# Performance work log

Hardware: AMD Instinct MI355X
Metric: run time of the kernel (lower is better)

The kernel has to match this reference:

```python
import jax, jax.numpy as jnp
import numpy as np

N_HEADS = 16
HEAD_SIZE = 64
N_EMB = 1024
BLOCK = 2048
B, T = 2, 2048

def setup_inputs() -> dict:
    key = jax.random.key(0)
    ks = jax.random.split(key, 6)
    s = 0.02
    x = jax.random.normal(ks[0], (B, T, N_EMB), dtype=jnp.float32)
    # per-head projection weights, stacked: [H, C, hs] (no bias, per module)
    Wq = jax.random.normal(ks[1], (N_HEADS, N_EMB, HEAD_SIZE), dtype=jnp.float32) * s
    Wk = jax.random.normal(ks[2], (N_HEADS, N_EMB, HEAD_SIZE), dtype=jnp.float32) * s
    Wv = jax.random.normal(ks[3], (N_HEADS, N_EMB, HEAD_SIZE), dtype=jnp.float32) * s
    # output projection: Linear(n_heads*head_size -> n_embedding), with bias
    Wo = jax.random.normal(ks[4], (N_HEADS * HEAD_SIZE, N_EMB), dtype=jnp.float32) * s
    bo = jax.random.normal(ks[5], (N_EMB,), dtype=jnp.float32) * s
    return {"x": x, "Wq": Wq, "Wk": Wk, "Wv": Wv, "Wo": Wo, "bo": bo}

def reference(x, Wq, Wk, Wv, Wo, bo):
    # x: [B,T,C]; projections per head -> [B,H,T,hs]
    q = jnp.einsum('btc,hcd->bhtd', x, Wq)
    k = jnp.einsum('btc,hcd->bhtd', x, Wk)
    v = jnp.einsum('btc,hcd->bhtd', x, Wv)
    scale = 1.0 / jnp.sqrt(jnp.asarray(HEAD_SIZE, dtype=x.dtype))
    scores = jnp.einsum('bhtd,bhsd->bhts', q, k) * scale  # [B,H,T,T]
    Tq = x.shape[1]
    causal = jnp.tril(jnp.ones((Tq, Tq), dtype=bool))
    scores = jnp.where(causal, scores, jnp.asarray(-jnp.inf, dtype=scores.dtype))
    attn = jax.nn.softmax(scores, axis=-1)  # dropout in eval mode (identity)
    out = jnp.einsum('bhts,bhsd->bhtd', attn, v)  # [B,H,T,hs]
    # concat heads along last dim (matches torch.cat order over head list)
    out = out.transpose(0, 2, 1, 3).reshape(x.shape[0], Tq, N_HEADS * HEAD_SIZE)
    return out @ Wo + bo
```

## Files before the change

### kernel.cpp

```cpp
#include <hip/hip_runtime.h>


typedef short v8s __attribute__((ext_vector_type(8)));
typedef float v4f __attribute__((ext_vector_type(4)));

#define DEVI __device__ __forceinline__

#define B_SZ 2
#define T_SEQ 2048
#define NH 16
#define HS 64
#define CEMB 1024
#define MROWS (B_SZ * T_SEQ)
#define KSZ 1024
#define SCALE_Q 0.18033688011112042f

DEVI unsigned short f2bf(float f) {
  union { float f; unsigned u; } c; c.f = f;
  unsigned u = c.u;
  unsigned r = (u + 0x7FFFu + ((u >> 16) & 1u)) >> 16;
  return (unsigned short)r;
}

DEVI float exp2_fast(float x) {
  float r;
  asm("v_exp_f32 %0, %1" : "=v"(r) : "v"(x));
  return r;
}

DEVI unsigned cvt_pk_bf16(float lo, float hi) {
  unsigned r;
  asm("v_cvt_pk_bf16_f32 %0, %1, %2" : "=v"(r) : "v"(lo), "v"(hi));
  return r;
}

DEVI void gload_lds16(const void* g, void* l) {
  __builtin_amdgcn_global_load_lds(
      (const __attribute__((address_space(1))) void*)g,
      (__attribute__((address_space(3))) void*)l, 16, 0, 0);
}

DEVI int xcd_swz(int bid, int nwg) {
  int q = nwg >> 3;
  return (bid & 7) * q + (bid >> 3);
}

__global__ __launch_bounds__(256, 4) void prep_kernel(
    const float* __restrict__ x, const float* __restrict__ Wq,
    const float* __restrict__ Wk, const float* __restrict__ Wv,
    const float* __restrict__ Wo, unsigned short* __restrict__ xb,
    unsigned short* __restrict__ Wt, unsigned short* __restrict__ Wot) {
  int bid = blockIdx.x;
  if (bid < 2048) {
    int i = bid * 2048 + threadIdx.x * 8;
    float4 a = *(const float4*)(x + i);
    float4 b = *(const float4*)(x + i + 4);
    ushort4 o0, o1;
    o0.x = f2bf(a.x); o0.y = f2bf(a.y); o0.z = f2bf(a.z); o0.w = f2bf(a.w);
    o1.x = f2bf(b.x); o1.y = f2bf(b.y); o1.z = f2bf(b.z); o1.w = f2bf(b.w);
    *(ushort4*)(xb + i) = o0;
    *(ushort4*)(xb + i + 4) = o1;
    return;
  }
  __shared__ float tile[32][33];
  const float* in; unsigned short* out;
  int C, bx, by;
  if (bid < 5120) {
    int b2 = bid - 2048;
    int widx = b2 >> 10, rem = b2 & 1023;
    in = (widx == 0 ? Wq : (widx == 1 ? Wk : Wv));
    int z = rem >> 6;
    bx = rem & 1; by = (rem >> 1) & 31;
    C = 64;
    in += (size_t)z * 1024 * 64;
    out = Wt + ((size_t)widx << 20) + (size_t)z * 1024 * 64;
  } else {
    int rem = bid - 5120;
    C = 1024;
    bx = rem & 31; by = rem >> 5;
    in = Wo; out = Wot;
  }
  int c0 = bx * 32, r0 = by * 32;
  int tx = threadIdx.x & 31, ty = threadIdx.x >> 5;
#pragma unroll
  for (int j = 0; j < 4; ++j)
    tile[ty + j * 8][tx] = in[(size_t)(r0 + ty + j * 8) * C + c0 + tx];
  __syncthreads();
#pragma unroll
  for (int j = 0; j < 4; ++j)
    out[(size_t)(c0 + ty + j * 8) * 1024 + r0 + tx] = f2bf(tile[tx][ty + j * 8]);
}

__global__ __launch_bounds__(256, 3) void gemm_qkv(
    const unsigned short* __restrict__ A, const unsigned short* __restrict__ Bt,
    unsigned short* __restrict__ Cout, int nbx) {
  __shared__ __align__(16) unsigned char lds[49152];
  unsigned short* As = (unsigned short*)lds;
  unsigned short* Bs = (unsigned short*)(lds + 24576);

  const int tid = threadIdx.x;
  const int lane = tid & 63, w = tid >> 6;
  const int wm = w >> 1, wn = w & 1;
  const int lr = lane & 15, lg = lane >> 4;

  const int wg = xcd_swz(blockIdx.x, gridDim.x);
  const int mb = (wg / nbx) * 128, nb = (wg % nbx) * 128;

  v4f acc[4][4];
  v4f zero = {0.f, 0.f, 0.f, 0.f};
#pragma unroll
  for (int i = 0; i < 4; ++i)
#pragma unroll
    for (int j = 0; j < 4; ++j) acc[i][j] = zero;

  const int srow = lane >> 2;
  const int sgcol = ((lane & 3) ^ (srow & 3)) * 8;
  const unsigned short* gA = A + (size_t)(mb + w * 32 + srow) * KSZ + sgcol;
  const unsigned short* gB = Bt + (size_t)(nb + w * 32 + srow) * KSZ + sgcol;
  unsigned short* lA = As + w * 1024;
  unsigned short* lB = Bs + w * 1024;

#define STAGE_G(buf, kb)                                        \
  do {                                                          \
    gload_lds16(gA + (kb), lA + (buf) * 4096);                  \
    gload_lds16(gA + (kb) + 16 * KSZ, lA + (buf) * 4096 + 512); \
    gload_lds16(gB + (kb), lB + (buf) * 4096);                  \
    gload_lds16(gB + (kb) + 16 * KSZ, lB + (buf) * 4096 + 512); \
  } while (0)

  STAGE_G(0, 0);
  STAGE_G(1, 32);
  STAGE_G(2, 64);

  const int NT = KSZ / 32;
  for (int t = 0; t < NT; ++t) {
    if (t < NT - 2)
      asm volatile("s_waitcnt vmcnt(8)" ::: "memory");
    else if (t == NT - 2)
      asm volatile("s_waitcnt vmcnt(4)" ::: "memory");
    else
      asm volatile("s_waitcnt vmcnt(0)" ::: "memory");
    __builtin_amdgcn_s_barrier();

    const int buf = t % 3;
    v8s af[4], bfr[4];
#pragma unroll
    for (int i = 0; i < 4; ++i) {
      int ra = wm * 64 + i * 16 + lr, rb = wn * 64 + i * 16 + lr;
      af[i]  = *(const v8s*)&As[buf * 4096 + ra * 32 + ((lg ^ (lr & 3)) << 3)];
      bfr[i] = *(const v8s*)&Bs[buf * 4096 + rb * 32 + ((lg ^ (lr & 3)) << 3)];
    }
#pragma unroll
    for (int i = 0; i < 4; ++i)
#pragma unroll
      for (int j = 0; j < 4; ++j)
        acc[i][j] = __builtin_amdgcn_mfma_f32_16x16x32_bf16(af[i], bfr[j], acc[i][j], 0, 0, 0);

    asm volatile("s_waitcnt lgkmcnt(0)" ::: "memory");
    __builtin_amdgcn_s_barrier();
    if (t + 3 < NT) STAGE_G(buf, (t + 3) * 32);
  }
#undef STAGE_G

  if ((wg % nbx) >= 16) {
    unsigned short* out = (unsigned short*)Cout;
#pragma unroll
    for (int i = 0; i < 4; ++i) {
      int tl0 = wm * 64 + i * 16 + lg * 4;
      int tc = tl0 >> 3, off = (tl0 & 7) * 2;
#pragma unroll
      for (int j = 0; j < 4; ++j) {
        int dl = wn * 64 + j * 16 + lr;
        unsigned lo = cvt_pk_bf16(acc[i][j][0], acc[i][j][1]);
        unsigned hi = cvt_pk_bf16(acc[i][j][2], acc[i][j][3]);
        unsigned char* p = lds + dl * 256 + ((tc ^ (dl & 15)) << 4) + off;
        *(unsigned*)p = lo;
        *(unsigned*)(p + 4) = hi;
      }
    }
    __syncthreads();
    int b = mb >> 11, mt = mb & 2047;
    int nrem0 = nb & 1023;
    unsigned short* Vg = out + (size_t)(2 * B_SZ * NH) * T_SEQ * HS;
#pragma unroll
    for (int it = 0; it < 8; ++it) {
      int dl = it * 16 + (tid >> 4);
      int tc = tid & 15;
      const unsigned char* p = lds + dl * 256 + ((tc ^ (dl & 15)) << 4);
      int4 vv = *(const int4*)p;
      int nrem = nrem0 + dl;
      int h = nrem >> 6, dd = nrem & 63;
      *(int4*)(Vg + ((size_t)(b * NH + h) * HS + dd) * T_SEQ + mt + tc * 8) = vv;
    }
    return;
  }

#pragma unroll
  for (int i = 0; i < 4; ++i) {
    int mrow0 = mb + wm * 64 + i * 16 + lg * 4;
#pragma unroll
    for (int j = 0; j < 4; ++j) {
      int ncol = nb + wn * 64 + j * 16 + lr;
      int p = ncol >> 10, rem = ncol & 1023, h = rem >> 6, d = rem & 63;
      float sc = (p == 0) ? SCALE_Q : 1.0f;
      unsigned short* out = (unsigned short*)Cout;
#pragma unroll
      for (int r = 0; r < 4; ++r) {
        int mrow = mrow0 + r;
        int b = mrow >> 11, t = mrow & 2047;
        out[((size_t)((p * B_SZ + b) * NH + h) * T_SEQ + t) * HS + d] =
            f2bf(acc[i][j][r] * sc);
      }
    }
  }
}

__global__ __launch_bounds__(256, 4) void gemm_proj(
    const unsigned short* __restrict__ A, const unsigned short* __restrict__ Bt,
    float* __restrict__ Cout, const float* __restrict__ bias, int nbx) {
  __shared__ __align__(16) unsigned short As[3][64 * 32];
  __shared__ __align__(16) unsigned short Bs[3][128 * 32];

  const int tid = threadIdx.x;
  const int lane = tid & 63, w = tid >> 6;
  const int wm = w >> 1, wn = w & 1;
  const int lr = lane & 15, lg = lane >> 4;

  const int wg = xcd_swz(blockIdx.x, gridDim.x);
  const int mb = (wg / nbx) * 64, nb = (wg % nbx) * 128;

  v4f acc[2][4];
  v4f zero = {0.f, 0.f, 0.f, 0.f};
#pragma unroll
  for (int i = 0; i < 2; ++i)
#pragma unroll
    for (int j = 0; j < 4; ++j) acc[i][j] = zero;

  const int srow = lane >> 2;
  const int sgcol = ((lane & 3) ^ (srow & 3)) * 8;
  const unsigned short* gA = A + (size_t)(mb + w * 16 + srow) * KSZ + sgcol;
  const unsigned short* gB = Bt + (size_t)(nb + w * 32 + srow) * KSZ + sgcol;
  unsigned short* lA = &As[0][0] + w * 512;
  unsigned short* lB = &Bs[0][0] + w * 1024;

#define STAGE_P(buf, kb)                                        \
  do {                                                          \
    gload_lds16(gA + (kb), lA + (buf) * 2048);                  \
    gload_lds16(gB + (kb), lB + (buf) * 4096);                  \
    gload_lds16(gB + (kb) + 16 * KSZ, lB + (buf) * 4096 + 512); \
  } while (0)

  STAGE_P(0, 0);
  STAGE_P(1, 32);
  STAGE_P(2, 64);

  const int NT = KSZ / 32;
  for (int t = 0; t < NT; ++t) {
    if (t < NT - 2)
      asm volatile("s_waitcnt vmcnt(6)" ::: "memory");
    else if (t == NT - 2)
      asm volatile("s_waitcnt vmcnt(3)" ::: "memory");
    else
      asm volatile("s_waitcnt vmcnt(0)" ::: "memory");
    __builtin_amdgcn_s_barrier();

    const int buf = t % 3;
    v8s af[2], bfr[4];
#pragma unroll
    for (int i = 0; i < 2; ++i) {
      int ra = wm * 32 + i * 16 + lr;
      af[i] = *(const v8s*)&As[buf][ra * 32 + ((lg ^ (lr & 3)) << 3)];
    }
#pragma unroll
    for (int j = 0; j < 4; ++j) {
      int rb = wn * 64 + j * 16 + lr;
      bfr[j] = *(const v8s*)&Bs[buf][rb * 32 + ((lg ^ (lr & 3)) << 3)];
    }
#pragma unroll
    for (int i = 0; i < 2; ++i)
#pragma unroll
      for (int j = 0; j < 4; ++j)
        acc[i][j] = __builtin_amdgcn_mfma_f32_16x16x32_bf16(af[i], bfr[j], acc[i][j], 0, 0, 0);

    asm volatile("s_waitcnt lgkmcnt(0)" ::: "memory");
    __builtin_amdgcn_s_barrier();
    if (t + 3 < NT) STAGE_P(buf, (t + 3) * 32);
  }
#undef STAGE_P

#pragma unroll
  for (int i = 0; i < 2; ++i) {
    int mrow0 = mb + wm * 32 + i * 16 + lg * 4;
#pragma unroll
    for (int j = 0; j < 4; ++j) {
      int ncol = nb + wn * 64 + j * 16 + lr;
      float bv = bias[ncol];
#pragma unroll
      for (int r = 0; r < 4; ++r)
        Cout[(size_t)(mrow0 + r) * CEMB + ncol] = acc[i][j][r] + bv;
    }
  }
}

__global__ __launch_bounds__(256, 4) void attn_kernel(
    const unsigned short* __restrict__ Qg, const unsigned short* __restrict__ Kg,
    const unsigned short* __restrict__ Vtg, unsigned short* __restrict__ Yg) {
  __shared__ __align__(16) unsigned char lds[32 * 1024];
  unsigned char* KsB = lds;
  unsigned char* VtB = lds + 16384;

  const int tid = threadIdx.x;
  const int lane = tid & 63, w = tid >> 6;
  const int lr = lane & 15, lg = lane >> 4;
  const int qc = 31 - (blockIdx.x >> 5);
  const int bh = blockIdx.x & 31;

  const unsigned short* Qbase = Qg + (size_t)bh * T_SEQ * HS;
  const unsigned short* Kbase = Kg + (size_t)bh * T_SEQ * HS;
  const unsigned short* Vtbase = Vtg + (size_t)bh * T_SEQ * HS;

  const int ks_row = tid >> 1, ks_c0 = (tid & 1) * 4;
  const unsigned short* Kg0 = Kbase + ks_row * HS + ks_c0 * 8;
  const int vs_d = tid >> 3, m0 = (tid & 7) * 2;
  const int vbt0 = ((m0 >> 2) << 4) + ((m0 & 3) << 2);
  const unsigned short* Vg0 = Vtbase + (size_t)vs_d * T_SEQ + vbt0;

  v8s qA[2];
  {
    const unsigned short* qrow = Qbase + (size_t)(qc * 64 + w * 16 + lr) * HS;
    qA[0] = *(const v8s*)(qrow + lg * 8);
    qA[1] = *(const v8s*)(qrow + 32 + lg * 8);
  }

  v4f O[4];
  v4f zero = {0.f, 0.f, 0.f, 0.f};
#pragma unroll
  for (int d = 0; d < 4; ++d) O[d] = zero;
  float mrun = -1e30f, lrun = 0.f;

  const int td = qc >> 1, oddq = qc & 1;

  int4 kA0 = ((const int4*)Kg0)[0], kA1 = ((const int4*)Kg0)[1];
  int4 kA2 = ((const int4*)Kg0)[2], kA3 = ((const int4*)Kg0)[3];
  int4 vl0 = *(const int4*)(Vg0);
  int4 vh0 = *(const int4*)(Vg0 + 64);
  int4 vl1 = *(const int4*)(Vg0 + 32 * T_SEQ);
  int4 vh1 = *(const int4*)(Vg0 + 32 * T_SEQ + 64);

  for (int t = 0; t <= td; ++t) {
    __syncthreads();
    {
      unsigned char* kp = KsB + ks_row * 128;
      *(int4*)(kp + (((ks_c0 + 0) ^ (ks_row & 7)) << 4)) = kA0;
      *(int4*)(kp + (((ks_c0 + 1) ^ (ks_row & 7)) << 4)) = kA1;
      *(int4*)(kp + (((ks_c0 + 2) ^ (ks_row & 7)) << 4)) = kA2;
      *(int4*)(kp + (((ks_c0 + 3) ^ (ks_row & 7)) << 4)) = kA3;
      int4 w0; w0.x = vl0.x; w0.y = vl0.y; w0.z = vh0.x; w0.w = vh0.y;
      int4 w1; w1.x = vl0.z; w1.y = vl0.w; w1.z = vh0.z; w1.w = vh0.w;
      unsigned char* vp = VtB + vs_d * 256;
      *(int4*)(vp + ((m0 ^ (vs_d & 15)) << 4)) = w0;
      *(int4*)(vp + (((m0 + 1) ^ (vs_d & 15)) << 4)) = w1;
      int4 w2; w2.x = vl1.x; w2.y = vl1.y; w2.z = vh1.x; w2.w = vh1.y;
      int4 w3; w3.x = vl1.z; w3.y = vl1.w; w3.z = vh1.z; w3.w = vh1.w;
      *(int4*)(vp + 8192 + ((m0 ^ (vs_d & 15)) << 4)) = w2;
      *(int4*)(vp + 8192 + (((m0 + 1) ^ (vs_d & 15)) << 4)) = w3;
    }
    __syncthreads();
    if (t < td) {
      const unsigned short* kp = Kg0 + (t + 1) * 8192;
      kA0 = ((const int4*)kp)[0]; kA1 = ((const int4*)kp)[1];
      kA2 = ((const int4*)kp)[2]; kA3 = ((const int4*)kp)[3];
      const unsigned short* vp = Vg0 + (t + 1) * 128;
      vl0 = *(const int4*)(vp);
      vh0 = *(const int4*)(vp + 64);
      vl1 = *(const int4*)(vp + 32 * T_SEQ);
      vh1 = *(const int4*)(vp + 32 * T_SEQ + 64);
    }

    const bool diag = (t == td);
    const int cflim = diag ? (oddq ? w + 4 : w) : 7;

    v4f S[8];
    __builtin_amdgcn_s_setprio(1);
#pragma unroll
    for (int cf = 0; cf < 8; ++cf) {
      if (cf <= cflim) {
        S[cf] = zero;
#pragma unroll
        for (int ks = 0; ks < 2; ++ks) {
          int srow = cf * 16 + lr;
          v8s kb = *(const v8s*)(KsB + srow * 128 +
                                 ((((ks << 2) + lg) ^ (lr & 7)) << 4));
          S[cf] = __builtin_amdgcn_mfma_f32_16x16x32_bf16(kb, qA[ks], S[cf], 0, 0, 0);
        }
      } else {
        S[cf] = (v4f){-1e30f, -1e30f, -1e30f, -1e30f};
      }
    }
    __builtin_amdgcn_s_setprio(0);

    if (diag) {
#pragma unroll
      for (int cf = 0; cf < 8; ++cf)
        if (cf == cflim) {
#pragma unroll
          for (int r = 0; r < 4; ++r)
            if (lg * 4 + r > lr) S[cf][r] = -1e30f;
        }
    }

    float mx = -1e30f;
#pragma unroll
    for (int cf = 0; cf < 8; ++cf)
#pragma unroll
      for (int r = 0; r < 4; ++r) mx = fmaxf(mx, S[cf][r]);
    mx = fmaxf(mx, __shfl_xor(mx, 16));
    mx = fmaxf(mx, __shfl_xor(mx, 32));

    if (!__all(mx - mrun <= 8.0f)) {
      float mn = fmaxf(mrun, mx);
      float alpha = exp2_fast(mrun - mn);
      mrun = mn;
      lrun *= alpha;
#pragma unroll
      for (int df = 0; df < 4; ++df)
#pragma unroll
        for (int r = 0; r < 4; ++r) O[df][r] *= alpha;
    }

    float sum = 0.f;
#pragma unroll
    for (int cf = 0; cf < 8; ++cf)
#pragma unroll
      for (int r = 0; r < 4; ++r) {
        float p = exp2_fast(S[cf][r] - mrun);
        S[cf][r] = p;
        sum += p;
      }
    sum += __shfl_xor(sum, 16);
    sum += __shfl_xor(sum, 32);
    lrun += sum;

    unsigned pk0[8], pk1[8];
#pragma unroll
    for (int cf = 0; cf < 8; ++cf) {
      pk0[cf] = cvt_pk_bf16(S[cf][0], S[cf][1]);
      pk1[cf] = cvt_pk_bf16(S[cf][2], S[cf][3]);
    }

    __builtin_amdgcn_s_setprio(1);
#pragma unroll
    for (int c = 0; c < 4; ++c) {
      if (!diag || oddq || c <= w) {
        union { unsigned u[4]; v8s s; } pu;
        pu.u[0] = pk0[c]; pu.u[1] = pk1[c];
        pu.u[2] = pk0[c + 4]; pu.u[3] = pk1[c + 4];
        v8s pa = pu.s;
#pragma unroll
        for (int df = 0; df < 4; ++df) {
          int d = df * 16 + lr;
          v8s va = *(const v8s*)(VtB + d * 256 +
                                 ((((c << 2) + lg) ^ lr) << 4));
          O[df] = __builtin_amdgcn_mfma_f32_16x16x32_bf16(va, pa, O[df], 0, 0, 0);
        }
      }
    }
    __builtin_amdgcn_s_setprio(0);
  }

  float invl = 1.0f / lrun;
  int tq = qc * 64 + w * 16 + lr;
  int b = bh >> 4, h = bh & 15;
  size_t ybase = ((size_t)b * T_SEQ + tq) * (NH * HS) + h * 64;
#pragma unroll
  for (int df = 0; df < 4; ++df) {
    ushort4 o4;
    o4.x = f2bf(O[df][0] * invl);
    o4.y = f2bf(O[df][1] * invl);
    o4.z = f2bf(O[df][2] * invl);
    o4.w = f2bf(O[df][3] * invl);
    *(ushort4*)(Yg + ybase + df * 16 + lg * 4) = o4;
  }
}

extern "C" void kernel_launch(void* const* d_in, const int* in_sizes, int n_in,
                              void* d_out, int out_size, void* d_ws, size_t ws_size,
                              hipStream_t stream) {
  (void)in_sizes; (void)n_in; (void)out_size; (void)ws_size;
  const float* x  = (const float*)d_in[0];
  const float* Wq = (const float*)d_in[1];
  const float* Wk = (const float*)d_in[2];
  const float* Wv = (const float*)d_in[3];
  const float* Wo = (const float*)d_in[4];
  const float* bo = (const float*)d_in[5];

  unsigned char* ws = (unsigned char*)d_ws;
  unsigned short* xb  = (unsigned short*)(ws);
  unsigned short* Wt  = (unsigned short*)(ws + (8u << 20));
  unsigned short* Wot = (unsigned short*)(ws + (14u << 20));
  unsigned short* qkv = (unsigned short*)(ws + (16u << 20));
  unsigned short* Y   = (unsigned short*)(ws + (40u << 20));

  prep_kernel<<<dim3(6144), 256, 0, stream>>>(x, Wq, Wk, Wv, Wo, xb, Wt, Wot);

  gemm_qkv<<<dim3(768), 256, 0, stream>>>(xb, Wt, qkv, 24);

  const unsigned short* Qp = qkv;
  const unsigned short* Kp = qkv + (size_t)B_SZ * NH * T_SEQ * HS;
  const unsigned short* Vtp = qkv + (size_t)2 * B_SZ * NH * T_SEQ * HS;
  attn_kernel<<<dim3(1024), 256, 0, stream>>>(Qp, Kp, Vtp, Y);

  gemm_proj<<<dim3(512), 256, 0, stream>>>(Y, Wot, (float*)d_out, bo, 8);
}
```

Before: 111.5 us.

## Use 128-row query tiles with 512-thread attention blocks and interleaved scheduling

```diff
diff --git a/kernel.cpp b/kernel.cpp
--- a/kernel.cpp
+++ b/kernel.cpp
@@ -302,7 +302,7 @@
   }
 }
 
-__global__ __launch_bounds__(256, 4) void attn_kernel(
+__global__ __launch_bounds__(512, 4) void attn_kernel(
     const unsigned short* __restrict__ Qg, const unsigned short* __restrict__ Kg,
     const unsigned short* __restrict__ Vtg, unsigned short* __restrict__ Yg) {
   __shared__ __align__(16) unsigned char lds[32 * 1024];
@@ -312,22 +312,25 @@
   const int tid = threadIdx.x;
   const int lane = tid & 63, w = tid >> 6;
   const int lr = lane & 15, lg = lane >> 4;
-  const int qc = 31 - (blockIdx.x >> 5);
+  const int kk = blockIdx.x >> 5;
+  const int qc = (kk & 1) ? (kk >> 1) : (15 - (kk >> 1));
   const int bh = blockIdx.x & 31;
 
   const unsigned short* Qbase = Qg + (size_t)bh * T_SEQ * HS;
   const unsigned short* Kbase = Kg + (size_t)bh * T_SEQ * HS;
   const unsigned short* Vtbase = Vtg + (size_t)bh * T_SEQ * HS;
 
-  const int ks_row = tid >> 1, ks_c0 = (tid & 1) * 4;
-  const unsigned short* Kg0 = Kbase + ks_row * HS + ks_c0 * 8;
-  const int vs_d = tid >> 3, m0 = (tid & 7) * 2;
-  const int vbt0 = ((m0 >> 2) << 4) + ((m0 & 3) << 2);
-  const unsigned short* Vg0 = Vtbase + (size_t)vs_d * T_SEQ + vbt0;
+  const int ks_row = tid >> 3, ks_cb = tid & 7;
+  const int kLds0 = ks_row * 128 + ((ks_cb ^ (ks_row & 7)) << 4);
+  const unsigned short* Kg0 = Kbase + ks_row * HS + ks_cb * 8;
+  const int vs_d = tid >> 4, vs_m = tid & 15;
+  const int vLds0 = vs_d * 256 + ((vs_m ^ (vs_d & 15)) << 4);
+  const int vbt = ((vs_m >> 2) << 4) + ((vs_m & 3) << 2);
+  const unsigned short* Vg0 = Vtbase + (size_t)vs_d * T_SEQ + vbt;
 
   v8s qA[2];
   {
-    const unsigned short* qrow = Qbase + (size_t)(qc * 64 + w * 16 + lr) * HS;
+    const unsigned short* qrow = Qbase + (size_t)(qc * 128 + w * 16 + lr) * HS;
     qA[0] = *(const v8s*)(qrow + lg * 8);
     qA[1] = *(const v8s*)(qrow + 32 + lg * 8);
   }
@@ -338,47 +341,36 @@
   for (int d = 0; d < 4; ++d) O[d] = zero;
   float mrun = -1e30f, lrun = 0.f;
 
-  const int td = qc >> 1, oddq = qc & 1;
-
-  int4 kA0 = ((const int4*)Kg0)[0], kA1 = ((const int4*)Kg0)[1];
-  int4 kA2 = ((const int4*)Kg0)[2], kA3 = ((const int4*)Kg0)[3];
-  int4 vl0 = *(const int4*)(Vg0);
-  int4 vh0 = *(const int4*)(Vg0 + 64);
-  int4 vl1 = *(const int4*)(Vg0 + 32 * T_SEQ);
-  int4 vh1 = *(const int4*)(Vg0 + 32 * T_SEQ + 64);
-
-  for (int t = 0; t <= td; ++t) {
+  int4 gK0 = *(const int4*)(Kg0);
+  int4 gK1 = *(const int4*)(Kg0 + 4096);
+  int2 vlo0 = *(const int2*)(Vg0);
+  int2 vhi0 = *(const int2*)(Vg0 + 64);
+  int2 vlo1 = *(const int2*)(Vg0 + 32 * T_SEQ);
+  int2 vhi1 = *(const int2*)(Vg0 + 32 * T_SEQ + 64);
+
+  for (int t = 0; t <= qc; ++t) {
     __syncthreads();
+    *(int4*)(KsB + kLds0) = gK0;
+    *(int4*)(KsB + kLds0 + 8192) = gK1;
     {
-      unsigned char* kp = KsB + ks_row * 128;
-      *(int4*)(kp + (((ks_c0 + 0) ^ (ks_row & 7)) << 4)) = kA0;
-      *(int4*)(kp + (((ks_c0 + 1) ^ (ks_row & 7)) << 4)) = kA1;
-      *(int4*)(kp + (((ks_c0 + 2) ^ (ks_row & 7)) << 4)) = kA2;
-      *(int4*)(kp + (((ks_c0 + 3) ^ (ks_row & 7)) << 4)) = kA3;
-      int4 w0; w0.x = vl0.x; w0.y = vl0.y; w0.z = vh0.x; w0.w = vh0.y;
-      int4 w1; w1.x = vl0.z; w1.y = vl0.w; w1.z = vh0.z; w1.w = vh0.w;
-      unsigned char* vp = VtB + vs_d * 256;
-      *(int4*)(vp + ((m0 ^ (vs_d & 15)) << 4)) = w0;
-      *(int4*)(vp + (((m0 + 1) ^ (vs_d & 15)) << 4)) = w1;
-      int4 w2; w2.x = vl1.x; w2.y = vl1.y; w2.z = vh1.x; w2.w = vh1.y;
-      int4 w3; w3.x = vl1.z; w3.y = vl1.w; w3.z = vh1.z; w3.w = vh1.w;
-      *(int4*)(vp + 8192 + ((m0 ^ (vs_d & 15)) << 4)) = w2;
-      *(int4*)(vp + 8192 + (((m0 + 1) ^ (vs_d & 15)) << 4)) = w3;
+      int4 v0; v0.x = vlo0.x; v0.y = vlo0.y; v0.z = vhi0.x; v0.w = vhi0.y;
+      int4 v1; v1.x = vlo1.x; v1.y = vlo1.y; v1.z = vhi1.x; v1.w = vhi1.y;
+      *(int4*)(VtB + vLds0) = v0;
+      *(int4*)(VtB + vLds0 + 8192) = v1;
     }
     __syncthreads();
-    if (t < td) {
-      const unsigned short* kp = Kg0 + (t + 1) * 8192;
-      kA0 = ((const int4*)kp)[0]; kA1 = ((const int4*)kp)[1];
-      kA2 = ((const int4*)kp)[2]; kA3 = ((const int4*)kp)[3];
+    if (t < qc) {
+      const unsigned short* kp = Kg0 + (t + 1) * (128 * HS);
+      gK0 = *(const int4*)kp;
+      gK1 = *(const int4*)(kp + 4096);
       const unsigned short* vp = Vg0 + (t + 1) * 128;
-      vl0 = *(const int4*)(vp);
-      vh0 = *(const int4*)(vp + 64);
-      vl1 = *(const int4*)(vp + 32 * T_SEQ);
-      vh1 = *(const int4*)(vp + 32 * T_SEQ + 64);
-    }
-
-    const bool diag = (t == td);
-    const int cflim = diag ? (oddq ? w + 4 : w) : 7;
+      vlo0 = *(const int2*)(vp);
+      vhi0 = *(const int2*)(vp + 64);
+      vlo1 = *(const int2*)(vp + 32 * T_SEQ);
+      vhi1 = *(const int2*)(vp + 32 * T_SEQ + 64);
+    }
+
+    const int cflim = (t == qc) ? w : 7;
 
     v4f S[8];
     __builtin_amdgcn_s_setprio(1);
@@ -399,10 +391,10 @@
     }
     __builtin_amdgcn_s_setprio(0);
 
-    if (diag) {
+    if (t == qc) {
 #pragma unroll
       for (int cf = 0; cf < 8; ++cf)
-        if (cf == cflim) {
+        if (cf == w) {
 #pragma unroll
           for (int r = 0; r < 4; ++r)
             if (lg * 4 + r > lr) S[cf][r] = -1e30f;
@@ -451,7 +443,7 @@
     __builtin_amdgcn_s_setprio(1);
 #pragma unroll
     for (int c = 0; c < 4; ++c) {
-      if (!diag || oddq || c <= w) {
+      if (t != qc || c <= w) {
         union { unsigned u[4]; v8s s; } pu;
         pu.u[0] = pk0[c]; pu.u[1] = pk1[c];
         pu.u[2] = pk0[c + 4]; pu.u[3] = pk1[c + 4];
@@ -469,7 +461,7 @@
   }
 
   float invl = 1.0f / lrun;
-  int tq = qc * 64 + w * 16 + lr;
+  int tq = qc * 128 + w * 16 + lr;
   int b = bh >> 4, h = bh & 15;
   size_t ybase = ((size_t)b * T_SEQ + tq) * (NH * HS) + h * 64;
 #pragma unroll
@@ -508,7 +500,7 @@
   const unsigned short* Qp = qkv;
   const unsigned short* Kp = qkv + (size_t)B_SZ * NH * T_SEQ * HS;
   const unsigned short* Vtp = qkv + (size_t)2 * B_SZ * NH * T_SEQ * HS;
-  attn_kernel<<<dim3(1024), 256, 0, stream>>>(Qp, Kp, Vtp, Y);
+  attn_kernel<<<dim3(512), 512, 0, stream>>>(Qp, Kp, Vtp, Y);
 
   gemm_proj<<<dim3(512), 256, 0, stream>>>(Y, Wot, (float*)d_out, bo, 8);
 }
```

After: 102.3 us. -8.3%, faster.
